# Kernel tuning notes

Hardware: AMD Instinct MI355X
Metric: run time of the kernel (lower is better)

The kernel has to match this reference:

```python
import jax, jax.numpy as jnp
import numpy as np

L = 4          # stack_size
H = 1024       # hidden_size
N = 16         # num_heads
D = H // N     # size_per_head = 64
F = 4096       # filter_size
B = 2
QLEN = 512
MLEN = 512
CLEN = QLEN + MLEN    # 1024
RLEN = CLEN + QLEN    # 1536
NEG_INF = -1e30
LN_EPS = 1e-12


def setup_inputs() -> dict:
    key = jax.random.key(0)
    ks = jax.random.split(key, 24)
    s = 0.02
    inp = {
        'content_stream': jax.random.normal(ks[0], (B, QLEN, H), jnp.float32),
        'content_mask': jnp.zeros((B, 1, QLEN, CLEN), jnp.float32),
        'position_encoding': jax.random.normal(ks[1], (B, RLEN, H), jnp.float32),
        'segment_matrix': jax.random.randint(ks[2], (B, QLEN, CLEN), 0, 2).astype(bool),
        'mems': jax.random.normal(ks[3], (L, B, MLEN, H), jnp.float32),
        # per-layer attention projection weights [L, H, N, D]
        'w_q': jax.random.normal(ks[4], (L, H, N, D), jnp.float32) * s,
        'w_k': jax.random.normal(ks[5], (L, H, N, D), jnp.float32) * s,
        'w_v': jax.random.normal(ks[6], (L, H, N, D), jnp.float32) * s,
        'w_r': jax.random.normal(ks[7], (L, H, N, D), jnp.float32) * s,
        'w_o': jax.random.normal(ks[8], (L, H, N, D), jnp.float32) * s,
        # FFN
        'ffn_w1': jax.random.normal(ks[9], (L, H, F), jnp.float32) * s,
        'ffn_b1': jnp.zeros((L, F), jnp.float32),
        'ffn_w2': jax.random.normal(ks[10], (L, F, H), jnp.float32) * s,
        'ffn_b2': jnp.zeros((L, H), jnp.float32),
        # LayerNorms (post-attn and post-ffn)
        'ln1_gamma': jnp.ones((L, H), jnp.float32),
        'ln1_beta': jnp.zeros((L, H), jnp.float32),
        'ln2_gamma': jnp.ones((L, H), jnp.float32),
        'ln2_beta': jnp.zeros((L, H), jnp.float32),
        # tied biases [N, D] and per-layer segment encoding [L, 2, N, D]
        'content_bias': jax.random.normal(ks[11], (N, D), jnp.float32) * H ** -0.5,
        'position_bias': jax.random.normal(ks[12], (N, D), jnp.float32) * H ** -0.5,
        'segment_bias': jax.random.normal(ks[13], (N, D), jnp.float32) * H ** -0.5,
        'segment_encoding': jax.random.normal(ks[14], (L, 2, N, D), jnp.float32) * H ** -0.5,
    }
    return inp


def _rel_shift(x, klen):
    # x: [b, n, q, r] -> rel-shifted and sliced to [b, n, q, klen]
    b, n, q, r = x.shape
    x = x.reshape(b, n, r, q)[:, :, 1:, :]
    x = x.reshape(b, n, q, r - 1)[:, :, :, :klen]
    return x


def _layernorm(x, gamma, beta):
    mu = jnp.mean(x, axis=-1, keepdims=True)
    var = jnp.mean(jnp.square(x - mu), axis=-1, keepdims=True)
    return (x - mu) * jax.lax.rsqrt(var + LN_EPS) * gamma + beta


def _forward(content_stream, content_mask, position_encoding, segment_matrix,
             mems, w_q, w_k, w_v, w_r, w_o, ffn_w1, ffn_b1, ffn_w2, ffn_b2,
             ln1_gamma, ln1_beta, ln2_gamma, ln2_beta,
             content_bias, position_bias, segment_bias, segment_encoding):
    x = content_stream
    seg = segment_matrix[:, None, :, :]  # [b,1,q,c]
    for l in range(L):
        context = jnp.concatenate([mems[l], x], axis=1)  # [b,c,h]
        q = jnp.einsum('bih,hnd->bind', x, w_q[l])
        k = jnp.einsum('bjh,hnd->bjnd', context, w_k[l])
        v = jnp.einsum('bjh,hnd->bjnd', context, w_v[l])
        r = jnp.einsum('brh,hnd->brnd', position_encoding, w_r[l])
        # content term
        ac = jnp.einsum('bind,bjnd->bnij', q + content_bias, k)
        # position term with rel-shift trick
        bd = jnp.einsum('bind,brnd->bnir', q + position_bias, r)
        bd = _rel_shift(bd, CLEN)
        # segment term: s in {0: different, 1: same-ish binary indicator}
        ef2 = jnp.einsum('bind,snd->bnis', q + segment_bias, segment_encoding[l])
        ef = jnp.where(seg, ef2[..., 1:2], ef2[..., 0:1])  # [b,n,q,c]
        scores = (ac + bd + ef) * (D ** -0.5)
        scores = scores + content_mask * NEG_INF  # mask==1 -> blocked
        probs = jax.nn.softmax(scores, axis=-1)
        attn = jnp.einsum('bnij,bjnd->bind', probs, v)
        attn_out = jnp.einsum('bind,hnd->bih', attn, w_o[l])
        # post-LN residual blocks (dropout is identity at inference)
        y = _layernorm(attn_out + x, ln1_gamma[l], ln1_beta[l])
        ffn = jnp.maximum(y @ ffn_w1[l] + ffn_b1[l], 0.0) @ ffn_w2[l] + ffn_b2[l]
        x = _layernorm(ffn + y, ln2_gamma[l], ln2_beta[l])
    return x


def reference(content_stream, content_mask, position_encoding, segment_matrix,
              mems, w_q, w_k, w_v, w_r, w_o, ffn_w1, ffn_b1, ffn_w2, ffn_b2,
              ln1_gamma, ln1_beta, ln2_gamma, ln2_beta,
              content_bias, position_bias, segment_bias, segment_encoding):
    return _forward(content_stream, content_mask, position_encoding,
                    segment_matrix, mems, w_q, w_k, w_v, w_r, w_o,
                    ffn_w1, ffn_b1, ffn_w2, ffn_b2,
                    ln1_gamma, ln1_beta, ln2_gamma, ln2_beta,
                    content_bias, position_bias, segment_bias, segment_encoding)
```

## Files before the change

### kernel.cpp

```cpp
#include <hip/hip_runtime.h>
#include <hip/hip_bf16.h>


#define BQ 2
#define QL 512
#define ML 512
#define CL 1024
#define RL 1536
#define HD 1024
#define NH 16
#define DH 64
#define FF 4096
#define NLAYER 4

typedef const float* FP;
typedef const __hip_bfloat16* BP;
typedef unsigned short u16;
typedef unsigned long long u64;
typedef __attribute__((ext_vector_type(8))) __bf16 bf16x8;
typedef __attribute__((ext_vector_type(4))) float f32x4;

static __device__ __forceinline__ float b2f(__hip_bfloat16 x) { return __bfloat162float(x); }
static __device__ __forceinline__ u16 f2u(float f) {
    union { __hip_bfloat16 h; u16 u; } c; c.h = __float2bfloat16(f); return c.u;
}
static __device__ __forceinline__ float u2f(u16 u) {
    union { float f; unsigned int i; } c; c.i = ((unsigned int)u) << 16; return c.f;
}

static __device__ __forceinline__ void gll16(const u16* g, u16* l) {
    __builtin_amdgcn_global_load_lds(
        (__attribute__((address_space(1))) void*)(u16*)g,
        (__attribute__((address_space(3))) void*)l, 16, 0, 0);
}

__global__ void sniff_kernel(const unsigned int* __restrict__ ln1_gamma,
                             const unsigned char* __restrict__ seg,
                             int* __restrict__ flags) {
    if (threadIdx.x == 0) {
        flags[0] = (ln1_gamma[0] == 0x3F800000u) ? 1 : 0;
        int int32ok = 1;
        for (int i = 0; i < 256; ++i)
            if ((i & 3) != 0 && seg[i] != 0) { int32ok = 0; break; }
        flags[1] = int32ok;
    }
}

__global__ void canon_kernel(FP inf, BP inb, u16* __restrict__ out,
                             int n, const int* __restrict__ flags) {
    int i = blockIdx.x * 256 + threadIdx.x;
    if (i >= n) return;
    out[i] = flags[0] ? f2u(inf[i]) : ((const u16*)inb)[i];
}

__global__ void out_write_kernel(const u16* __restrict__ in, void* __restrict__ out,
                                 int n, const int* __restrict__ flags) {
    int i = blockIdx.x * 256 + threadIdx.x;
    if (i >= n) return;
    if (flags[0]) ((float*)out)[i] = u2f(in[i]);
    else          ((u16*)out)[i] = in[i];
}

__global__ __launch_bounds__(256) void segmask_packT_kernel(
    const void* __restrict__ seg, FP maskf, BP maskb,
    u16* __restrict__ maskT, const int* __restrict__ flags) {
    __shared__ u16 t[32][33];
    const int tid = threadIdx.x;
    const int j0 = blockIdx.x * 32, i0 = blockIdx.y * 32, b = blockIdx.z;
    const int tc = tid & 31, tr = tid >> 5;
    const int f32 = flags[0], s32 = flags[1];
    #pragma unroll
    for (int p = 0; p < 4; ++p) {
        int i = i0 + p * 8 + tr;
        size_t gi = ((size_t)(b * QL + i)) * CL + j0 + tc;
        int sv = s32 ? ((const int*)seg)[gi] : (int)((const signed char*)seg)[gi];
        float mk = f32 ? maskf[gi] : b2f(maskb[gi]);
        t[p * 8 + tr][tc] = (u16)((f2u(mk * -1e30f) & 0xFFFEu) | (sv ? 1u : 0u));
    }
    __syncthreads();
    #pragma unroll
    for (int p = 0; p < 4; ++p) {
        int j = j0 + p * 8 + tr;
        maskT[((size_t)(b * CL + j)) * QL + i0 + tc] = t[tc][p * 8 + tr];
    }
}

__global__ __launch_bounds__(256) void transpose_kernel(
    FP inf, BP inb, u16* __restrict__ out, int R, int Cc,
    const int* __restrict__ flags) {
    __shared__ float t[32][33];
    const int tid = threadIdx.x;
    const int c0 = blockIdx.x * 32, r0 = blockIdx.y * 32;
    const int tc = tid & 31, tr = tid >> 5;
    const int f32 = flags[0];
    #pragma unroll
    for (int p = 0; p < 4; ++p) {
        int r = r0 + p * 8 + tr;
        size_t gi = (size_t)r * Cc + c0 + tc;
        t[p * 8 + tr][tc] = f32 ? inf[gi] : b2f(inb[gi]);
    }
    __syncthreads();
    #pragma unroll
    for (int p = 0; p < 4; ++p) {
        int c = c0 + p * 8 + tr;
        out[(size_t)c * R + r0 + tc] = f2u(t[tc][p * 8 + tr]);
    }
}

__global__ __launch_bounds__(256) void vtrans_kernel(
    const u16* __restrict__ Vb, u16* __restrict__ VT) {
    __shared__ u16 t[32][33];
    const int tid = threadIdx.x;
    const int j0 = blockIdx.x * 32, d0 = blockIdx.y * 32, bn = blockIdx.z;
    const int b = bn >> 4, n = bn & 15;
    const int tc = tid & 31, tr = tid >> 5;
    #pragma unroll
    for (int p = 0; p < 4; ++p) {
        int j = j0 + p * 8 + tr;
        t[p * 8 + tr][tc] = Vb[((size_t)(b * CL + j) * NH + n) * DH + d0 + tc];
    }
    __syncthreads();
    #pragma unroll
    for (int p = 0; p < 4; ++p) {
        int d = d0 + p * 8 + tr;
        VT[((size_t)bn * DH + d) * CL + j0 + tc] = t[tc][p * 8 + tr];
    }
}

__global__ void build_ctx_kernel(FP memf, BP memb, const u16* __restrict__ X,
                                 u16* __restrict__ CTX, const int* __restrict__ flags) {
    int i = blockIdx.x * 256 + threadIdx.x;
    int h = i % HD;
    int r = (i / HD) % CL;
    int b = i / (HD * CL);
    if (r < ML) {
        size_t mi = ((size_t)(b * ML + r)) * HD + h;
        CTX[i] = flags[0] ? f2u(memf[mi]) : ((const u16*)memb)[mi];
    } else {
        CTX[i] = X[((size_t)(b * QL + (r - ML))) * HD + h];
    }
}

__device__ __forceinline__ void gemm128_core(
    const u16* __restrict__ A, int lda, const u16* __restrict__ Bt, int ldb,
    int K, int tid, u16* sA, u16* sB, f32x4 (&acc)[4][4])
{
    const int lane = tid & 63, w = tid >> 6;
    const int wm = (w & 1) * 64, wn = (w >> 1) * 64;
    const int lr = lane & 15, quad = lane >> 4;
    const int srow = lane >> 2;
    const int sch = (lane & 3) * 8;

    for (int k0 = 0; k0 < K; k0 += 32) {
        #pragma unroll
        for (int j = 0; j < 2; ++j) {
            int rb = w * 32 + j * 16;
            gll16(&A[(size_t)(rb + srow) * lda + k0 + sch], &sA[rb * 32 + lane * 8]);
            gll16(&Bt[(size_t)(rb + srow) * ldb + k0 + sch], &sB[rb * 32 + lane * 8]);
        }
        __syncthreads();
        bf16x8 af[4], bf[4];
        #pragma unroll
        for (int mi = 0; mi < 4; ++mi)
            af[mi] = *(const bf16x8*)&sA[(wm + mi * 16 + lr) * 32 + quad * 8];
        #pragma unroll
        for (int ni = 0; ni < 4; ++ni)
            bf[ni] = *(const bf16x8*)&sB[(wn + ni * 16 + lr) * 32 + quad * 8];
        #pragma unroll
        for (int mi = 0; mi < 4; ++mi)
            #pragma unroll
            for (int ni = 0; ni < 4; ++ni)
                acc[mi][ni] = __builtin_amdgcn_mfma_f32_16x16x32_bf16(
                    af[mi], bf[ni], acc[mi][ni], 0, 0, 0);
        __syncthreads();
    }
}

#define ACC_INIT(acc) \
    _Pragma("unroll") for (int mi = 0; mi < 4; ++mi) \
        _Pragma("unroll") for (int ni = 0; ni < 4; ++ni) \
            acc[mi][ni] = (f32x4){0.f, 0.f, 0.f, 0.f};

__global__ __launch_bounds__(256) void proj4_gemm(
    const u16* __restrict__ X, const u16* __restrict__ CTX,
    const u16* __restrict__ PE, const u16* __restrict__ W4,
    u16* __restrict__ Qb, u16* __restrict__ Kb,
    u16* __restrict__ Vb, u16* __restrict__ Rb)
{
    __shared__ __align__(16) u16 sA[128 * 32];
    __shared__ __align__(16) u16 sB[128 * 32];
    const int tid = threadIdx.x;
    const int by = blockIdx.y;
    const u16* Abase; u16* Cbase; int seg, mb;
    if (by < 8)       { seg = 0; Abase = X;   Cbase = Qb; mb = by; }
    else if (by < 24) { seg = 1; Abase = CTX; Cbase = Kb; mb = by - 8; }
    else if (by < 40) { seg = 2; Abase = CTX; Cbase = Vb; mb = by - 24; }
    else              { seg = 3; Abase = PE;  Cbase = Rb; mb = by - 40; }
    const int m0 = mb * 128, n0 = blockIdx.x * 128;

    f32x4 acc[4][4];
    ACC_INIT(acc)
    gemm128_core(Abase + (size_t)m0 * HD, HD,
                 W4 + (size_t)seg * HD * HD + (size_t)n0 * HD, HD, HD,
                 tid, sA, sB, acc);

    const int lane = tid & 63, w = tid >> 6;
    const int wm = (w & 1) * 64, wn = (w >> 1) * 64;
    const int lr = lane & 15, quad = lane >> 4;
    #pragma unroll
    for (int ni = 0; ni < 4; ++ni) {
        int col = n0 + wn + ni * 16 + lr;
        #pragma unroll
        for (int mi = 0; mi < 4; ++mi) {
            int row = m0 + wm + mi * 16 + quad * 4;
            #pragma unroll
            for (int r = 0; r < 4; ++r)
                Cbase[(size_t)(row + r) * HD + col] = f2u(acc[mi][ni][r]);
        }
    }
}

__global__ __launch_bounds__(256) void gemm128_splitk(
    const u16* __restrict__ A, const u16* __restrict__ Bt,
    float* __restrict__ part, int N, int Kfull, int Kc, size_t zstride)
{
    __shared__ __align__(16) u16 sA[128 * 32];
    __shared__ __align__(16) u16 sB[128 * 32];
    const int tid = threadIdx.x;
    const int n0 = blockIdx.x * 128, m0 = blockIdx.y * 128, z = blockIdx.z;
    f32x4 acc[4][4];
    ACC_INIT(acc)
    gemm128_core(A + (size_t)m0 * Kfull + z * Kc, Kfull,
                 Bt + (size_t)n0 * Kfull + z * Kc, Kfull, Kc,
                 tid, sA, sB, acc);

    float* P = part + (size_t)z * zstride;
    const int lane = tid & 63, w = tid >> 6;
    const int wm = (w & 1) * 64, wn = (w >> 1) * 64;
    const int lr = lane & 15, quad = lane >> 4;
    #pragma unroll
    for (int ni = 0; ni < 4; ++ni) {
        int col = n0 + wn + ni * 16 + lr;
        #pragma unroll
        for (int mi = 0; mi < 4; ++mi) {
            int row = m0 + wm + mi * 16 + quad * 4;
            #pragma unroll
            for (int r = 0; r < 4; ++r)
                P[(size_t)(row + r) * N + col] = acc[mi][ni][r];
        }
    }
}

template <bool HASBIAS, int NPART>
__global__ __launch_bounds__(256) void reduce_add_ln(
    const float* __restrict__ part, FP biasf, BP biasb,
    const u16* __restrict__ resid, FP gf, BP gb, FP bef, BP beb,
    u16* __restrict__ O, const int* __restrict__ flags)
{
    const int row = blockIdx.x;
    const int tid = threadIdx.x;
    const int wid = tid >> 6, lane = tid & 63;
    __shared__ float r1[4], r2[4];
    const int f32 = flags[0];
    float v[4];
    #pragma unroll
    for (int c = 0; c < 4; ++c) {
        int h = c * 256 + tid;
        size_t idx = (size_t)row * HD + h;
        float s = 0.f;
        #pragma unroll
        for (int k = 0; k < NPART; ++k)
            s += part[idx + (size_t)k * 1048576];
        if (HASBIAS) s += f32 ? biasf[h] : b2f(biasb[h]);
        v[c] = s + u2f(resid[idx]);
    }
    float s = v[0] + v[1] + v[2] + v[3];
    #pragma unroll
    for (int o = 32; o > 0; o >>= 1) s += __shfl_xor(s, o);
    if (lane == 0) r1[wid] = s;
    __syncthreads();
    float mu = (r1[0] + r1[1] + r1[2] + r1[3]) * (1.0f / HD);
    float q = 0.f;
    #pragma unroll
    for (int c = 0; c < 4; ++c) { float d = v[c] - mu; q += d * d; }
    #pragma unroll
    for (int o = 32; o > 0; o >>= 1) q += __shfl_xor(q, o);
    if (lane == 0) r2[wid] = q;
    __syncthreads();
    float var = (r2[0] + r2[1] + r2[2] + r2[3]) * (1.0f / HD);
    float inv = rsqrtf(var + 1e-12f);
    #pragma unroll
    for (int c = 0; c < 4; ++c) {
        int h = c * 256 + tid;
        float g = f32 ? gf[h] : b2f(gb[h]);
        float be = f32 ? bef[h] : b2f(beb[h]);
        O[(size_t)row * HD + h] = f2u((v[c] - mu) * inv * g + be);
    }
}

__global__ __launch_bounds__(256) void reduce_bias_relu_kernel(
    const float* __restrict__ part, FP b1f, BP b1b,
    u16* __restrict__ Out, const int* __restrict__ flags)
{
    const int g = blockIdx.x * 256 + threadIdx.x;
    const float4 p0 = ((const float4*)part)[g];
    const float4 p1 = ((const float4*)(part + 4194304))[g];
    const int col = (g * 4) & (FF - 1);
    const int f32 = flags[0];
    ushort4 o;
    #pragma unroll
    for (int j = 0; j < 4; ++j) {
        float bv = f32 ? b1f[col + j] : b2f(b1b[col + j]);
        float v = (&p0.x)[j] + (&p1.x)[j] + bv;
        (&o.x)[j] = f2u(fmaxf(v, 0.0f));
    }
    ((ushort4*)Out)[g] = o;
}

__global__ void ef2_kernel(const u16* __restrict__ Qb, FP sbf, BP sbb,
                           FP sef, BP seb, float* __restrict__ EF,
                           const int* __restrict__ flags) {
    int t = blockIdx.x * 256 + threadIdx.x;
    if (t >= BQ * NH * QL) return;
    int i = t % QL;
    int n = (t / QL) % NH;
    int b = t / (QL * NH);
    float e0 = 0.f, e1 = 0.f;
    const int f32 = flags[0];
    for (int d = 0; d < DH; ++d) {
        float sbv = f32 ? sbf[n * DH + d] : b2f(sbb[n * DH + d]);
        float s0 = f32 ? sef[(0 * NH + n) * DH + d] : b2f(seb[(0 * NH + n) * DH + d]);
        float s1 = f32 ? sef[(1 * NH + n) * DH + d] : b2f(seb[(1 * NH + n) * DH + d]);
        float qv = u2f(Qb[((size_t)(b * QL + i) * NH + n) * DH + d]) + sbv;
        e0 += qv * s0;
        e1 += qv * s1;
    }
    EF[(size_t)t * 2 + 0] = e0;
    EF[(size_t)t * 2 + 1] = e1;
}

__global__ void ckpr_kernel(const u16* __restrict__ Kb, const u16* __restrict__ Rb,
                            FP cbf, BP cbb, FP pbf, BP pbb,
                            float* __restrict__ CK, float* __restrict__ PR,
                            const int* __restrict__ flags) {
    int t = blockIdx.x * 256 + threadIdx.x;
    const int f32 = flags[0];
    if (t < 32 * CL) {
        int bn = t >> 10, j = t & (CL - 1);
        int b = bn >> 4, n = bn & 15;
        float s = 0.f;
        for (int d = 0; d < DH; ++d) {
            float c = f32 ? cbf[n * DH + d] : b2f(cbb[n * DH + d]);
            s += c * u2f(Kb[((size_t)(b * CL + j) * NH + n) * DH + d]);
        }
        CK[t] = s;
    } else {
        int t2 = t - 32 * CL;
        if (t2 >= 32 * RL) return;
        int bn = t2 / RL, rr = t2 % RL;
        int b = bn >> 4, n = bn & 15;
        float s = 0.f;
        for (int d = 0; d < DH; ++d) {
            float c = f32 ? pbf[n * DH + d] : b2f(pbb[n * DH + d]);
            s += c * u2f(Rb[((size_t)(b * RL + rr) * NH + n) * DH + d]);
        }
        PR[(size_t)bn * RL + rr] = s;
    }
}

#define FA_SP 72
#define FA_SD 84
__global__ __launch_bounds__(256, 4) void flash_attn_kernel(
    const u16* __restrict__ Qb, const u16* __restrict__ Kb,
    const u16* __restrict__ Rb, const u16* __restrict__ VT,
    const float* __restrict__ CK, const float* __restrict__ PR,
    const float* __restrict__ EF,
    const u16* __restrict__ maskT, u16* __restrict__ AT)
{
    __shared__ __align__(16) u16 sP[4][16 * FA_SP];
    __shared__ __align__(16) float sD[4][16 * FA_SD];

    const int tid = threadIdx.x;
    const int w = tid >> 6;
    const int lane = tid & 63;
    const int lr = lane & 15, quad = lane >> 4;

    const int blin = blockIdx.x;
    const int xcd = blin & 7, slot = blin >> 3;
    const int bn = xcd + 8 * (slot >> 5);
    const int itile = slot & 31;
    const int b = bn >> 4, n = bn & 15;
    const int i0 = itile * 16;

    u16* myP = sP[w];
    float* myD = sD[w];

    const size_t qoff = ((size_t)(b * QL + i0 + lr) * NH + n) * DH + quad * 8;
    const bf16x8 q0 = *(const bf16x8*)&Qb[qoff];
    const bf16x8 q1 = *(const bf16x8*)&Qb[qoff + 32];

    float ef0[4], ef1[4];
    #pragma unroll
    for (int r = 0; r < 4; ++r) {
        size_t e = ((size_t)bn * QL + i0 + quad * 4 + r) * 2;
        ef0[r] = EF[e]; ef1[r] = EF[e + 1];
    }

    f32x4 accO[4];
    #pragma unroll
    for (int c = 0; c < 4; ++c) accO[c] = (f32x4){0.f, 0.f, 0.f, 0.f};
    float m[4], l[4];
    #pragma unroll
    for (int r = 0; r < 4; ++r) { m[r] = -1e38f; l[r] = 0.f; }

    #pragma unroll 1
    for (int t = 0; t < 4; ++t) {
        const int j0 = w * 64 + t * 256;
        const int base16 = 497 - i0 + j0;

        bf16x8 kf[8];
        const u16* kbase = &Kb[((size_t)(b * CL + j0 + lr) * NH + n) * DH + quad * 8];
        #pragma unroll
        for (int ct = 0; ct < 4; ++ct) {
            const u16* kp = kbase + (size_t)ct * 16 * (NH * DH);
            kf[ct * 2]     = *(const bf16x8*)kp;
            kf[ct * 2 + 1] = *(const bf16x8*)(kp + 32);
        }
        f32x4 acc[4];
        #pragma unroll
        for (int c = 0; c < 4; ++c) acc[c] = (f32x4){0.f, 0.f, 0.f, 0.f};
        #pragma unroll
        for (int ct = 0; ct < 4; ++ct) {
            acc[ct] = __builtin_amdgcn_mfma_f32_16x16x32_bf16(q0, kf[ct * 2], acc[ct], 0, 0, 0);
            acc[ct] = __builtin_amdgcn_mfma_f32_16x16x32_bf16(q1, kf[ct * 2 + 1], acc[ct], 0, 0, 0);
        }

        #pragma unroll
        for (int f = 0; f < 5; ++f) {
            int rr = base16 + f * 16 + lr;
            rr = rr > RL - 1 ? RL - 1 : rr;
            const u16* rp = &Rb[((size_t)(b * RL + rr) * NH + n) * DH + quad * 8];
            bf16x8 rf0 = *(const bf16x8*)rp;
            bf16x8 rf1 = *(const bf16x8*)(rp + 32);
            float prv = PR[(size_t)bn * RL + rr];
            f32x4 bd = (f32x4){0.f, 0.f, 0.f, 0.f};
            bd = __builtin_amdgcn_mfma_f32_16x16x32_bf16(q0, rf0, bd, 0, 0, 0);
            bd = __builtin_amdgcn_mfma_f32_16x16x32_bf16(q1, rf1, bd, 0, 0, 0);
            #pragma unroll
            for (int r = 0; r < 4; ++r)
                myD[(quad * 4 + r) * FA_SD + f * 16 + lr] = bd[r] + prv;
        }
        __syncthreads();

        bf16x8 vf[8];
        #pragma unroll
        for (int ct = 0; ct < 4; ++ct) {
            const u16* vp = &VT[((size_t)bn * DH + ct * 16 + lr) * CL + j0 + quad * 8];
            vf[ct * 2]     = *(const bf16x8*)vp;
            vf[ct * 2 + 1] = *(const bf16x8*)(vp + 32);
        }

        #pragma unroll
        for (int ct = 0; ct < 4; ++ct) {
            float ckv = CK[(size_t)bn * CL + j0 + ct * 16 + lr];
            u64 mq = *(const u64*)&maskT[((size_t)(b * CL + j0 + ct * 16 + lr)) * QL + i0 + quad * 4];
            #pragma unroll
            for (int r = 0; r < 4; ++r) {
                int ilw = quad * 4 + r;
                int p = 15 - ilw + ct * 16 + lr;
                float bdv = myD[ilw * FA_SD + p];
                u16 mv = (u16)(mq >> (16 * r));
                float efv = (mv & 1) ? ef1[r] : ef0[r];
                float mka = u2f((u16)(mv & 0xFFFEu));
                acc[ct][r] = (acc[ct][r] + bdv + ckv + efv) * 0.125f + mka;
            }
        }

        float a[4];
        #pragma unroll
        for (int r = 0; r < 4; ++r) {
            float tm = fmaxf(fmaxf(acc[0][r], acc[1][r]), fmaxf(acc[2][r], acc[3][r]));
            tm = fmaxf(tm, __shfl_xor(tm, 1));
            tm = fmaxf(tm, __shfl_xor(tm, 2));
            tm = fmaxf(tm, __shfl_xor(tm, 4));
            tm = fmaxf(tm, __shfl_xor(tm, 8));
            float mn = fmaxf(m[r], tm);
            a[r] = __expf(m[r] - mn);
            m[r] = mn;
        }
        float ts[4] = {0.f, 0.f, 0.f, 0.f};
        #pragma unroll
        for (int ct = 0; ct < 4; ++ct)
            #pragma unroll
            for (int r = 0; r < 4; ++r) {
                float pv = __expf(acc[ct][r] - m[r]);
                ts[r] += pv;
                myP[(quad * 4 + r) * FA_SP + ct * 16 + lr] = f2u(pv);
            }
        #pragma unroll
        for (int r = 0; r < 4; ++r) {
            float s = ts[r];
            s += __shfl_xor(s, 1);
            s += __shfl_xor(s, 2);
            s += __shfl_xor(s, 4);
            s += __shfl_xor(s, 8);
            l[r] = l[r] * a[r] + s;
            #pragma unroll
            for (int c = 0; c < 4; ++c) accO[c][r] *= a[r];
        }
        __syncthreads();

        const bf16x8 pa0 = *(const bf16x8*)&myP[lr * FA_SP + quad * 8];
        const bf16x8 pa1 = *(const bf16x8*)&myP[lr * FA_SP + 32 + quad * 8];
        #pragma unroll
        for (int ct = 0; ct < 4; ++ct) {
            accO[ct] = __builtin_amdgcn_mfma_f32_16x16x32_bf16(pa0, vf[ct * 2], accO[ct], 0, 0, 0);
            accO[ct] = __builtin_amdgcn_mfma_f32_16x16x32_bf16(pa1, vf[ct * 2 + 1], accO[ct], 0, 0, 0);
        }
    }
    __syncthreads();
    float* cmb = &sD[0][0];
    if (w != 0) {
        float* c = &cmb[((w - 1) * 64 + lane) * 25];
        #pragma unroll
        for (int ct = 0; ct < 4; ++ct)
            #pragma unroll
            for (int r = 0; r < 4; ++r) c[ct * 4 + r] = accO[ct][r];
        #pragma unroll
        for (int r = 0; r < 4; ++r) { c[16 + r] = m[r]; c[20 + r] = l[r]; }
    }
    __syncthreads();
    if (w == 0) {
        float M[4], es[4], eo[3][4], lt[4];
        #pragma unroll
        for (int r = 0; r < 4; ++r) M[r] = m[r];
        #pragma unroll
        for (int k = 0; k < 3; ++k) {
            const float* c = &cmb[(k * 64 + lane) * 25];
            #pragma unroll
            for (int r = 0; r < 4; ++r) M[r] = fmaxf(M[r], c[16 + r]);
        }
        #pragma unroll
        for (int r = 0; r < 4; ++r) { es[r] = __expf(m[r] - M[r]); lt[r] = l[r] * es[r]; }
        #pragma unroll
        for (int k = 0; k < 3; ++k) {
            const float* c = &cmb[(k * 64 + lane) * 25];
            #pragma unroll
            for (int r = 0; r < 4; ++r) {
                eo[k][r] = __expf(c[16 + r] - M[r]);
                lt[r] += c[20 + r] * eo[k][r];
            }
        }
        #pragma unroll
        for (int ct = 0; ct < 4; ++ct)
            #pragma unroll
            for (int r = 0; r < 4; ++r) {
                float o = accO[ct][r] * es[r];
                #pragma unroll
                for (int k = 0; k < 3; ++k)
                    o += cmb[(k * 64 + lane) * 25 + ct * 4 + r] * eo[k][r];
                AT[((size_t)(b * QL + i0 + quad * 4 + r) * NH + n) * DH + ct * 16 + lr]
                    = f2u(o / lt[r]);
            }
    }
}

extern "C" void kernel_launch(void* const* d_in, const int* in_sizes, int n_in,
                              void* d_out, int out_size, void* d_ws, size_t ws_size,
                              hipStream_t stream) {
    (void)in_sizes; (void)n_in; (void)out_size; (void)ws_size;
    const void* content_stream = d_in[0];
    const void* content_mask   = d_in[1];
    const void* pos_enc        = d_in[2];
    const void* seg_mat        = d_in[3];
    const void* mems           = d_in[4];
    const void* w_q            = d_in[5];
    const void* w_k            = d_in[6];
    const void* w_v            = d_in[7];
    const void* w_r            = d_in[8];
    const void* w_o            = d_in[9];
    const void* ffn_w1         = d_in[10];
    const void* ffn_b1         = d_in[11];
    const void* ffn_w2         = d_in[12];
    const void* ffn_b2         = d_in[13];
    const void* ln1_g          = d_in[14];
    const void* ln1_b          = d_in[15];
    const void* ln2_g          = d_in[16];
    const void* ln2_b          = d_in[17];
    const void* cb             = d_in[18];
    const void* pb             = d_in[19];
    const void* sb             = d_in[20];
    const void* se             = d_in[21];

    float* SC    = (float*)d_ws;
    float* PART  = SC + 4194304;
    float* EF    = SC + 16777216;
    float* CK    = EF + 32768;
    float* PR    = CK + 32768;
    int*   flags = (int*)(PR + 49152);
    u16*   bws   = (u16*)(flags + 16);

    u16* X   = bws;               u16* Y   = X   + 1048576;
    u16* CTX = Y   + 1048576;     u16* Qb  = CTX + 2097152;
    u16* Kb  = Qb  + 1048576;     u16* Vb  = Kb  + 2097152;
    u16* Rb  = Vb  + 2097152;     u16* PE  = Rb  + 3145728;
    u16* AT  = PE  + 3145728;
    u16* W4  = AT  + 1048576;
    u16* WOc = W4  + 4194304;     u16* W1T = WOc + 1048576;
    u16* W2T = W1T + 4194304;
    u16* F1  = (u16*)SC;
    u16* VT  = (u16*)(SC + 12582912);
    u16* maskT = (u16*)(SC + 13631488);

    const size_t wstride   = (size_t)HD * HD;
    const size_t memstride = (size_t)BQ * ML * HD;

    const dim3 blk(256);
    #define DUAL(base, off) ((FP)(base) + (off)), ((BP)(base) + (off))

    sniff_kernel<<<dim3(1), dim3(64), 0, stream>>>(
        (const unsigned int*)ln1_g, (const unsigned char*)seg_mat, flags);

    canon_kernel<<<dim3((BQ * QL * HD) / 256), blk, 0, stream>>>(
        DUAL(content_stream, 0), X, BQ * QL * HD, flags);
    canon_kernel<<<dim3((BQ * RL * HD) / 256), blk, 0, stream>>>(
        DUAL(pos_enc, 0), PE, BQ * RL * HD, flags);
    segmask_packT_kernel<<<dim3(CL / 32, QL / 32, BQ), blk, 0, stream>>>(
        seg_mat, DUAL(content_mask, 0), maskT, flags);

    for (int l = 0; l < NLAYER; ++l) {
        transpose_kernel<<<dim3(32, 32), blk, 0, stream>>>(
            DUAL(w_q, (size_t)l * wstride), W4, HD, HD, flags);
        transpose_kernel<<<dim3(32, 32), blk, 0, stream>>>(
            DUAL(w_k, (size_t)l * wstride), W4 + 1048576, HD, HD, flags);
        transpose_kernel<<<dim3(32, 32), blk, 0, stream>>>(
            DUAL(w_v, (size_t)l * wstride), W4 + 2097152, HD, HD, flags);
        transpose_kernel<<<dim3(32, 32), blk, 0, stream>>>(
            DUAL(w_r, (size_t)l * wstride), W4 + 3145728, HD, HD, flags);
        canon_kernel<<<dim3((HD * HD) / 256), blk, 0, stream>>>(
            DUAL(w_o, (size_t)l * wstride), WOc, HD * HD, flags);
        transpose_kernel<<<dim3(FF / 32, HD / 32), blk, 0, stream>>>(
            DUAL(ffn_w1, (size_t)l * HD * FF), W1T, HD, FF, flags);
        transpose_kernel<<<dim3(HD / 32, FF / 32), blk, 0, stream>>>(
            DUAL(ffn_w2, (size_t)l * FF * HD), W2T, FF, HD, flags);

        build_ctx_kernel<<<dim3((BQ * CL * HD) / 256), blk, 0, stream>>>(
            DUAL(mems, (size_t)l * memstride), X, CTX, flags);

        proj4_gemm<<<dim3(8, 64), blk, 0, stream>>>(
            X, CTX, PE, W4, Qb, Kb, Vb, Rb);

        ef2_kernel<<<dim3((BQ * NH * QL) / 256), blk, 0, stream>>>(
            Qb, DUAL(sb, 0), DUAL(se, (size_t)l * 2 * NH * DH), EF, flags);
        ckpr_kernel<<<dim3((32 * CL + 32 * RL) / 256), blk, 0, stream>>>(
            Kb, Rb, DUAL(cb, 0), DUAL(pb, 0), CK, PR, flags);
        vtrans_kernel<<<dim3(CL / 32, DH / 32, BQ * NH), blk, 0, stream>>>(Vb, VT);

        flash_attn_kernel<<<dim3(1024), blk, 0, stream>>>(
            Qb, Kb, Rb, VT, CK, PR, EF, maskT, AT);

        gemm128_splitk<<<dim3(8, 8, 8), blk, 0, stream>>>(
            AT, WOc, PART, HD, HD, 128, 1048576);
        reduce_add_ln<false, 8><<<dim3(BQ * QL), blk, 0, stream>>>(
            PART, (FP)nullptr, (BP)nullptr, X,
            DUAL(ln1_g, (size_t)l * HD), DUAL(ln1_b, (size_t)l * HD), Y, flags);

        gemm128_splitk<<<dim3(FF / 128, 8, 2), blk, 0, stream>>>(
            Y, W1T, PART, FF, HD, 512, 4194304);
        reduce_bias_relu_kernel<<<dim3(4096), blk, 0, stream>>>(
            PART, DUAL(ffn_b1, (size_t)l * FF), F1, flags);

        gemm128_splitk<<<dim3(8, 8, 8), blk, 0, stream>>>(
            F1, W2T, PART, HD, FF, 512, 1048576);
        reduce_add_ln<true, 8><<<dim3(BQ * QL), blk, 0, stream>>>(
            PART, DUAL(ffn_b2, (size_t)l * HD), Y,
            DUAL(ln2_g, (size_t)l * HD), DUAL(ln2_b, (size_t)l * HD), X, flags);
    }
    #undef DUAL

    out_write_kernel<<<dim3((BQ * QL * HD) / 256), blk, 0, stream>>>(
        X, d_out, BQ * QL * HD, flags);
}
```

Baseline: 1.220 ms.

## Fuse context build and V transpose into projection GEMM, batch weight transposes

Removes the per-layer build_ctx kernel by having the K/V projection read directly from a pre-converted bf16 mems buffer or X. It also writes V straight into transposed VT layout from the GEMM epilogue, which drops the separate vtrans kernel. The four Q/K/V/R weight transposes are merged into a single launch. The ef2 and ckpr dot products now use 16-byte vector loads. The cost is strided 8-byte stores in the V epilogue and an upfront conversion of all layers' mems.

```diff
diff --git a/kernel.cpp b/kernel.cpp
--- a/kernel.cpp
+++ b/kernel.cpp
@@ -18,6 +18,7 @@
 typedef unsigned short u16;
 typedef unsigned long long u64;
 typedef __attribute__((ext_vector_type(8))) __bf16 bf16x8;
+typedef __attribute__((ext_vector_type(8))) unsigned short u16x8;
 typedef __attribute__((ext_vector_type(4))) float f32x4;
 
 static __device__ __forceinline__ float b2f(__hip_bfloat16 x) { return __bfloat162float(x); }
@@ -107,37 +108,31 @@
     }
 }
 
-__global__ __launch_bounds__(256) void vtrans_kernel(
-    const u16* __restrict__ Vb, u16* __restrict__ VT) {
-    __shared__ u16 t[32][33];
+__global__ __launch_bounds__(256) void transpose4_kernel(
+    FP aqf, BP aqb, FP akf, BP akb, FP avf, BP avb, FP arf, BP arb,
+    u16* __restrict__ W4, const int* __restrict__ flags) {
+    __shared__ float t[32][33];
     const int tid = threadIdx.x;
-    const int j0 = blockIdx.x * 32, d0 = blockIdx.y * 32, bn = blockIdx.z;
-    const int b = bn >> 4, n = bn & 15;
+    const int c0 = blockIdx.x * 32, r0 = blockIdx.y * 32, z = blockIdx.z;
     const int tc = tid & 31, tr = tid >> 5;
+    const int f32 = flags[0];
+    FP inf; BP inb;
+    if (z == 0)      { inf = aqf; inb = aqb; }
+    else if (z == 1) { inf = akf; inb = akb; }
+    else if (z == 2) { inf = avf; inb = avb; }
+    else             { inf = arf; inb = arb; }
+    u16* out = W4 + (size_t)z * (HD * HD);
     #pragma unroll
     for (int p = 0; p < 4; ++p) {
-        int j = j0 + p * 8 + tr;
-        t[p * 8 + tr][tc] = Vb[((size_t)(b * CL + j) * NH + n) * DH + d0 + tc];
+        int r = r0 + p * 8 + tr;
+        size_t gi = (size_t)r * HD + c0 + tc;
+        t[p * 8 + tr][tc] = f32 ? inf[gi] : b2f(inb[gi]);
     }
     __syncthreads();
     #pragma unroll
     for (int p = 0; p < 4; ++p) {
-        int d = d0 + p * 8 + tr;
-        VT[((size_t)bn * DH + d) * CL + j0 + tc] = t[tc][p * 8 + tr];
-    }
-}
-
-__global__ void build_ctx_kernel(FP memf, BP memb, const u16* __restrict__ X,
-                                 u16* __restrict__ CTX, const int* __restrict__ flags) {
-    int i = blockIdx.x * 256 + threadIdx.x;
-    int h = i % HD;
-    int r = (i / HD) % CL;
-    int b = i / (HD * CL);
-    if (r < ML) {
-        size_t mi = ((size_t)(b * ML + r)) * HD + h;
-        CTX[i] = flags[0] ? f2u(memf[mi]) : ((const u16*)memb)[mi];
-    } else {
-        CTX[i] = X[((size_t)(b * QL + (r - ML))) * HD + h];
+        int c = c0 + p * 8 + tr;
+        out[(size_t)c * HD + r0 + tc] = f2u(t[tc][p * 8 + tr]);
     }
 }
 
@@ -182,40 +177,61 @@
             acc[mi][ni] = (f32x4){0.f, 0.f, 0.f, 0.f};
 
 __global__ __launch_bounds__(256) void proj4_gemm(
-    const u16* __restrict__ X, const u16* __restrict__ CTX,
+    const u16* __restrict__ X, const u16* __restrict__ memsL,
     const u16* __restrict__ PE, const u16* __restrict__ W4,
     u16* __restrict__ Qb, u16* __restrict__ Kb,
-    u16* __restrict__ Vb, u16* __restrict__ Rb)
+    u16* __restrict__ VT, u16* __restrict__ Rb)
 {
     __shared__ __align__(16) u16 sA[128 * 32];
     __shared__ __align__(16) u16 sB[128 * 32];
     const int tid = threadIdx.x;
     const int by = blockIdx.y;
-    const u16* Abase; u16* Cbase; int seg, mb;
-    if (by < 8)       { seg = 0; Abase = X;   Cbase = Qb; mb = by; }
-    else if (by < 24) { seg = 1; Abase = CTX; Cbase = Kb; mb = by - 8; }
-    else if (by < 40) { seg = 2; Abase = CTX; Cbase = Vb; mb = by - 24; }
-    else              { seg = 3; Abase = PE;  Cbase = Rb; mb = by - 40; }
+    const u16* Abase; u16* Cbase = nullptr; int seg, mb;
+    if (by < 8)       { seg = 0; mb = by;      Abase = X + (size_t)mb * 128 * HD; Cbase = Qb; }
+    else if (by < 24) { seg = 1; mb = by - 8;  Cbase = Kb; Abase = nullptr; }
+    else if (by < 40) { seg = 2; mb = by - 24; Abase = nullptr; }
+    else              { seg = 3; mb = by - 40; Abase = PE + (size_t)mb * 128 * HD; Cbase = Rb; }
+    if (seg == 1 || seg == 2) {
+        int b = mb >> 3, r0 = (mb & 7) * 128;
+        Abase = (r0 < ML) ? memsL + ((size_t)(b * ML + r0)) * HD
+                          : X + ((size_t)(b * QL + (r0 - ML))) * HD;
+    }
     const int m0 = mb * 128, n0 = blockIdx.x * 128;
 
     f32x4 acc[4][4];
     ACC_INIT(acc)
-    gemm128_core(Abase + (size_t)m0 * HD, HD,
-                 W4 + (size_t)seg * HD * HD + (size_t)n0 * HD, HD, HD,
+    gemm128_core(Abase, HD, W4 + (size_t)seg * HD * HD + (size_t)n0 * HD, HD, HD,
                  tid, sA, sB, acc);
 
     const int lane = tid & 63, w = tid >> 6;
     const int wm = (w & 1) * 64, wn = (w >> 1) * 64;
     const int lr = lane & 15, quad = lane >> 4;
-    #pragma unroll
-    for (int ni = 0; ni < 4; ++ni) {
-        int col = n0 + wn + ni * 16 + lr;
-        #pragma unroll
-        for (int mi = 0; mi < 4; ++mi) {
-            int row = m0 + wm + mi * 16 + quad * 4;
-            #pragma unroll
-            for (int r = 0; r < 4; ++r)
-                Cbase[(size_t)(row + r) * HD + col] = f2u(acc[mi][ni][r]);
+    if (seg != 2) {
+        #pragma unroll
+        for (int ni = 0; ni < 4; ++ni) {
+            int col = n0 + wn + ni * 16 + lr;
+            #pragma unroll
+            for (int mi = 0; mi < 4; ++mi) {
+                int row = m0 + wm + mi * 16 + quad * 4;
+                #pragma unroll
+                for (int r = 0; r < 4; ++r)
+                    Cbase[(size_t)(row + r) * HD + col] = f2u(acc[mi][ni][r]);
+            }
+        }
+    } else {
+        #pragma unroll
+        for (int ni = 0; ni < 4; ++ni) {
+            int col = n0 + wn + ni * 16 + lr;
+            int nh = col >> 6, d = col & 63;
+            #pragma unroll
+            for (int mi = 0; mi < 4; ++mi) {
+                int row = m0 + wm + mi * 16 + quad * 4;
+                int b = row >> 10, j = row & 1023;
+                ushort4 o;
+                #pragma unroll
+                for (int r = 0; r < 4; ++r) (&o.x)[r] = f2u(acc[mi][ni][r]);
+                *(ushort4*)&VT[(((size_t)(b * NH + nh) * DH + d) * CL + j)] = o;
+            }
         }
     }
 }
@@ -327,13 +343,19 @@
     int b = t / (QL * NH);
     float e0 = 0.f, e1 = 0.f;
     const int f32 = flags[0];
-    for (int d = 0; d < DH; ++d) {
-        float sbv = f32 ? sbf[n * DH + d] : b2f(sbb[n * DH + d]);
-        float s0 = f32 ? sef[(0 * NH + n) * DH + d] : b2f(seb[(0 * NH + n) * DH + d]);
-        float s1 = f32 ? sef[(1 * NH + n) * DH + d] : b2f(seb[(1 * NH + n) * DH + d]);
-        float qv = u2f(Qb[((size_t)(b * QL + i) * NH + n) * DH + d]) + sbv;
-        e0 += qv * s0;
-        e1 += qv * s1;
+    const u16* qrow = &Qb[((size_t)(b * QL + i) * NH + n) * DH];
+    for (int d0 = 0; d0 < DH; d0 += 8) {
+        u16x8 qv = *(const u16x8*)&qrow[d0];
+        #pragma unroll
+        for (int j = 0; j < 8; ++j) {
+            int d = d0 + j;
+            float sbv = f32 ? sbf[n * DH + d] : b2f(sbb[n * DH + d]);
+            float s0 = f32 ? sef[(0 * NH + n) * DH + d] : b2f(seb[(0 * NH + n) * DH + d]);
+            float s1 = f32 ? sef[(1 * NH + n) * DH + d] : b2f(seb[(1 * NH + n) * DH + d]);
+            float qv_f = u2f(qv[j]) + sbv;
+            e0 += qv_f * s0;
+            e1 += qv_f * s1;
+        }
     }
     EF[(size_t)t * 2 + 0] = e0;
     EF[(size_t)t * 2 + 1] = e1;
@@ -349,9 +371,15 @@
         int bn = t >> 10, j = t & (CL - 1);
         int b = bn >> 4, n = bn & 15;
         float s = 0.f;
-        for (int d = 0; d < DH; ++d) {
-            float c = f32 ? cbf[n * DH + d] : b2f(cbb[n * DH + d]);
-            s += c * u2f(Kb[((size_t)(b * CL + j) * NH + n) * DH + d]);
+        const u16* krow = &Kb[((size_t)(b * CL + j) * NH + n) * DH];
+        for (int d0 = 0; d0 < DH; d0 += 8) {
+            u16x8 kv = *(const u16x8*)&krow[d0];
+            #pragma unroll
+            for (int jj = 0; jj < 8; ++jj) {
+                int d = d0 + jj;
+                float c = f32 ? cbf[n * DH + d] : b2f(cbb[n * DH + d]);
+                s += c * u2f(kv[jj]);
+            }
         }
         CK[t] = s;
     } else {
@@ -360,9 +388,15 @@
         int bn = t2 / RL, rr = t2 % RL;
         int b = bn >> 4, n = bn & 15;
         float s = 0.f;
-        for (int d = 0; d < DH; ++d) {
-            float c = f32 ? pbf[n * DH + d] : b2f(pbb[n * DH + d]);
-            s += c * u2f(Rb[((size_t)(b * RL + rr) * NH + n) * DH + d]);
+        const u16* rrow = &Rb[((size_t)(b * RL + rr) * NH + n) * DH];
+        for (int d0 = 0; d0 < DH; d0 += 8) {
+            u16x8 rv = *(const u16x8*)&rrow[d0];
+            #pragma unroll
+            for (int jj = 0; jj < 8; ++jj) {
+                int d = d0 + jj;
+                float c = f32 ? pbf[n * DH + d] : b2f(pbb[n * DH + d]);
+                s += c * u2f(rv[jj]);
+            }
         }
         PR[(size_t)bn * RL + rr] = s;
     }
@@ -600,20 +634,19 @@
     int*   flags = (int*)(PR + 49152);
     u16*   bws   = (u16*)(flags + 16);
 
-    u16* X   = bws;               u16* Y   = X   + 1048576;
-    u16* CTX = Y   + 1048576;     u16* Qb  = CTX + 2097152;
-    u16* Kb  = Qb  + 1048576;     u16* Vb  = Kb  + 2097152;
-    u16* Rb  = Vb  + 2097152;     u16* PE  = Rb  + 3145728;
+    u16* MEMSB = bws;
+    u16* X   = MEMSB + 4194304;       u16* Y   = X   + 1048576;
+    u16* Qb  = Y   + 1048576;         u16* Kb  = Qb  + 1048576;
+    u16* Rb  = Kb  + 2097152;         u16* PE  = Rb  + 3145728;
     u16* AT  = PE  + 3145728;
     u16* W4  = AT  + 1048576;
-    u16* WOc = W4  + 4194304;     u16* W1T = WOc + 1048576;
+    u16* WOc = W4  + 4194304;         u16* W1T = WOc + 1048576;
     u16* W2T = W1T + 4194304;
     u16* F1  = (u16*)SC;
     u16* VT  = (u16*)(SC + 12582912);
     u16* maskT = (u16*)(SC + 13631488);
 
     const size_t wstride   = (size_t)HD * HD;
-    const size_t memstride = (size_t)BQ * ML * HD;
 
     const dim3 blk(256);
     #define DUAL(base, off) ((FP)(base) + (off)), ((BP)(base) + (off))
@@ -625,18 +658,16 @@
         DUAL(content_stream, 0), X, BQ * QL * HD, flags);
     canon_kernel<<<dim3((BQ * RL * HD) / 256), blk, 0, stream>>>(
         DUAL(pos_enc, 0), PE, BQ * RL * HD, flags);
+    canon_kernel<<<dim3((NLAYER * BQ * ML * HD) / 256), blk, 0, stream>>>(
+        DUAL(mems, 0), MEMSB, NLAYER * BQ * ML * HD, flags);
     segmask_packT_kernel<<<dim3(CL / 32, QL / 32, BQ), blk, 0, stream>>>(
         seg_mat, DUAL(content_mask, 0), maskT, flags);
 
     for (int l = 0; l < NLAYER; ++l) {
-        transpose_kernel<<<dim3(32, 32), blk, 0, stream>>>(
-            DUAL(w_q, (size_t)l * wstride), W4, HD, HD, flags);
-        transpose_kernel<<<dim3(32, 32), blk, 0, stream>>>(
-            DUAL(w_k, (size_t)l * wstride), W4 + 1048576, HD, HD, flags);
-        transpose_kernel<<<dim3(32, 32), blk, 0, stream>>>(
-            DUAL(w_v, (size_t)l * wstride), W4 + 2097152, HD, HD, flags);
-        transpose_kernel<<<dim3(32, 32), blk, 0, stream>>>(
-            DUAL(w_r, (size_t)l * wstride), W4 + 3145728, HD, HD, flags);
+        transpose4_kernel<<<dim3(32, 32, 4), blk, 0, stream>>>(
+            DUAL(w_q, (size_t)l * wstride), DUAL(w_k, (size_t)l * wstride),
+            DUAL(w_v, (size_t)l * wstride), DUAL(w_r, (size_t)l * wstride),
+            W4, flags);
         canon_kernel<<<dim3((HD * HD) / 256), blk, 0, stream>>>(
             DUAL(w_o, (size_t)l * wstride), WOc, HD * HD, flags);
         transpose_kernel<<<dim3(FF / 32, HD / 32), blk, 0, stream>>>(
@@ -644,17 +675,13 @@
         transpose_kernel<<<dim3(HD / 32, FF / 32), blk, 0, stream>>>(
             DUAL(ffn_w2, (size_t)l * FF * HD), W2T, FF, HD, flags);
 
-        build_ctx_kernel<<<dim3((BQ * CL * HD) / 256), blk, 0, stream>>>(
-            DUAL(mems, (size_t)l * memstride), X, CTX, flags);
-
         proj4_gemm<<<dim3(8, 64), blk, 0, stream>>>(
-            X, CTX, PE, W4, Qb, Kb, Vb, Rb);
+            X, MEMSB + (size_t)l * BQ * ML * HD, PE, W4, Qb, Kb, VT, Rb);
 
         ef2_kernel<<<dim3((BQ * NH * QL) / 256), blk, 0, stream>>>(
             Qb, DUAL(sb, 0), DUAL(se, (size_t)l * 2 * NH * DH), EF, flags);
         ckpr_kernel<<<dim3((32 * CL + 32 * RL) / 256), blk, 0, stream>>>(
             Kb, Rb, DUAL(cb, 0), DUAL(pb, 0), CK, PR, flags);
-        vtrans_kernel<<<dim3(CL / 32, DH / 32, BQ * NH), blk, 0, stream>>>(Vb, VT);
 
         flash_attn_kernel<<<dim3(1024), blk, 0, stream>>>(
             Qb, Kb, Rb, VT, CK, PR, EF, maskT, AT);
```

Measured after the change: 1.101 ms. 1.11x faster.
